# Kernel optimization log

Measured on AMD Instinct MI355X. Metric: run time of the kernel, lower is better.

## Reference

```python
import jax, jax.numpy as jnp
import numpy as np

H = 1024   # hidden_size
A = 16     # number_ab (branches)
O = 4      # num_outputs per branch
B = 4096   # batch
P = 2048   # number of selected rows
EPS = 1e-5


def setup_inputs() -> dict:
    key = jax.random.key(0)
    ks = jax.random.split(key, 12)
    s = 0.02  # weight init scale
    inp = {
        "X": jax.random.normal(ks[0], (B, H), jnp.float32),
        "X1": jax.random.normal(ks[1], (B, H), jnp.float32),
        # stacked per-branch parameters (batched over antibody axis A)
        "W1": jax.random.normal(ks[2], (A, H, H), jnp.float32) * s,
        "b1": jnp.zeros((A, H), jnp.float32),
        "W2": jax.random.normal(ks[3], (A, H, H), jnp.float32) * s,
        "b2": jnp.zeros((A, H), jnp.float32),
        "W3": jax.random.normal(ks[4], (A, H, H), jnp.float32) * s,
        "b3": jnp.zeros((A, H), jnp.float32),
        "gamma": jnp.ones((A, H), jnp.float32),
        "beta": jnp.zeros((A, H), jnp.float32),
        "W4": jax.random.normal(ks[5], (A, H, O), jnp.float32) * s,
        "b4": jnp.zeros((A, O), jnp.float32),
        "positions_y": jax.random.randint(ks[6], (P,), 0, B, jnp.int32),
    }
    return inp


def reference(X, X1, W1, b1, W2, b2, W3, b3, gamma, beta, W4, b4, positions_y):
    # z = l1(X) + l2(X1) per branch, batched over A: [B, A, H]
    z = (jnp.einsum('bh,aho->bao', X, W1) + b1
         + jnp.einsum('bh,aho->bao', X1, W2) + b2)
    # mlm: Linear -> ReLU -> LayerNorm -> Linear
    h = jax.nn.relu(jnp.einsum('bah,aho->bao', z, W3) + b3)  # [B, A, H]
    mu = jnp.mean(h, axis=-1, keepdims=True)
    var = jnp.var(h, axis=-1, keepdims=True)  # biased, matches nn.LayerNorm
    hn = (h - mu) / jnp.sqrt(var + EPS) * gamma + beta
    y = jnp.einsum('bah,aho->bao', hn, W4) + b4  # [B, A, O]
    # torch.cat along dim 1 over branches -> [B, A*O]
    Y = y.reshape(B, A * O)
    return Y[positions_y]
```

## Files before the change

### kernel.cpp

```cpp
#include <hip/hip_runtime.h>
#include <hip/hip_bf16.h>

using bf16 = __hip_bfloat16;
typedef __bf16 v8bf __attribute__((ext_vector_type(8)));
typedef float v4f __attribute__((ext_vector_type(4)));

#define H_ 1024
#define A_ 16
#define O_ 4
#define B_ 4096
#define P_ 2048
#define EPS_ 1e-5f

__device__ __forceinline__ void gl_lds16(const void* g, void* l) {
    __builtin_amdgcn_global_load_lds(
        (const __attribute__((address_space(1))) void*)g,
        (__attribute__((address_space(3))) void*)l, 16, 0, 0);
}

__global__ __launch_bounds__(256) void gather_bias_k(const float* __restrict__ X,
                                                     const float* __restrict__ X1,
                                                     const int* __restrict__ pos,
                                                     bf16* __restrict__ XX,
                                                     const float* __restrict__ b1,
                                                     const float* __restrict__ b2,
                                                     float* __restrict__ b12) {
    if (blockIdx.x >= P_) {
        int i = (blockIdx.x - P_) * 256 + threadIdx.x;
        if (i < A_ * H_) b12[i] = b1[i] + b2[i];
        return;
    }
    int p = blockIdx.x;
    int row = pos[p];
    const float4* x  = (const float4*)(X  + (size_t)row * H_);
    const float4* x1 = (const float4*)(X1 + (size_t)row * H_);
    bf16* o = XX + (size_t)p * (2 * H_);
    int i = threadIdx.x;
    float4 v = x[i];
    __align__(8) bf16 t[4];
    t[0] = __float2bfloat16(v.x); t[1] = __float2bfloat16(v.y);
    t[2] = __float2bfloat16(v.z); t[3] = __float2bfloat16(v.w);
    *(uint2*)(o + i * 4) = *(const uint2*)t;
    float4 w = x1[i];
    t[0] = __float2bfloat16(w.x); t[1] = __float2bfloat16(w.y);
    t[2] = __float2bfloat16(w.z); t[3] = __float2bfloat16(w.w);
    *(uint2*)(o + H_ + i * 4) = *(const uint2*)t;
}

__global__ __launch_bounds__(256) void transpose12_k(const float* __restrict__ W1s,
                                                     const float* __restrict__ W2s,
                                                     bf16* __restrict__ WT12) {
    __shared__ float tile[64][65];
    const int which = blockIdx.z >> 4;
    const int a = blockIdx.z & 15;
    const float* src = (which == 0) ? W1s : W2s;
    const int kOff = which * H_;

    const int k0 = blockIdx.x * 64;
    const int n0 = blockIdx.y * 64;
    const float* s = src + (size_t)a * H_ * H_;
    const int tc = threadIdx.x & 15;
    const int tr = threadIdx.x >> 4;
#pragma unroll
    for (int r = 0; r < 64; r += 16) {
        float4 v = *(const float4*)(s + (size_t)(k0 + tr + r) * H_ + n0 + tc * 4);
        tile[tr + r][tc * 4 + 0] = v.x;
        tile[tr + r][tc * 4 + 1] = v.y;
        tile[tr + r][tc * 4 + 2] = v.z;
        tile[tr + r][tc * 4 + 3] = v.w;
    }
    __syncthreads();
    bf16* d = WT12 + (size_t)a * H_ * (2 * H_) + kOff;
    const int wc = threadIdx.x & 7;
    const int wr = threadIdx.x >> 3;
#pragma unroll
    for (int r = 0; r < 64; r += 32) {
        const int n = wr + r;
        __align__(16) bf16 tmp[8];
#pragma unroll
        for (int j = 0; j < 8; j++) tmp[j] = __float2bfloat16(tile[wc * 8 + j][n]);
        *(uint4*)(d + (size_t)(n0 + n) * (2 * H_) + k0 + wc * 8) = *(const uint4*)tmp;
    }
}

template <bool RELU, bool FUSET3>
__global__ __launch_bounds__(256) void gemm_bt(const bf16* __restrict__ Amat, size_t aStrideA,
                                               const bf16* __restrict__ Bt,
                                               const float* __restrict__ bias,
                                               bf16* __restrict__ C,
                                               int M, int N, int K,
                                               const float* __restrict__ W3s,
                                               bf16* __restrict__ WT3d) {
    __shared__ __align__(16) char smem[32768];
    unsigned short* As = (unsigned short*)smem;
    unsigned short* Bs = (unsigned short*)(smem + 16384);

    const int L = blockIdx.x + 16 * blockIdx.y + 128 * blockIdx.z;

    if (FUSET3 && L >= 2048) {
        const int t = L - 2048;
        const int a = t >> 8;
        const int rem = t & 255;
        const int k0 = (rem & 15) * 64;
        const int n0 = (rem >> 4) * 64;
        float(*tile)[65] = (float(*)[65])smem;
        const float* s = W3s + (size_t)a * H_ * H_;
        const int tc = threadIdx.x & 15;
        const int tr = threadIdx.x >> 4;
#pragma unroll
        for (int r = 0; r < 64; r += 16) {
            float4 v = *(const float4*)(s + (size_t)(k0 + tr + r) * H_ + n0 + tc * 4);
            tile[tr + r][tc * 4 + 0] = v.x;
            tile[tr + r][tc * 4 + 1] = v.y;
            tile[tr + r][tc * 4 + 2] = v.z;
            tile[tr + r][tc * 4 + 3] = v.w;
        }
        __syncthreads();
        bf16* d = WT3d + (size_t)a * H_ * H_;
        const int wc = threadIdx.x & 7;
        const int wr = threadIdx.x >> 3;
#pragma unroll
        for (int r = 0; r < 64; r += 32) {
            const int n = wr + r;
            __align__(16) bf16 tmp[8];
#pragma unroll
            for (int j = 0; j < 8; j++) tmp[j] = __float2bfloat16(tile[wc * 8 + j][n]);
            *(uint4*)(d + (size_t)(n0 + n) * H_ + k0 + wc * 8) = *(const uint4*)tmp;
        }
        return;
    }

    const int xcd = L & 7;
    const int g = L >> 3;
    const int bm = g & 15;
    const int bna = xcd + 8 * (g >> 4);
    const int bn = bna & 7;
    const int a = bna >> 3;

    const bf16* Ab = Amat + (size_t)a * aStrideA;
    const bf16* Bb = Bt + (size_t)a * (size_t)N * K;
    const int tid = threadIdx.x;
    const int lane = tid & 63;
    const int wave = tid >> 6;
    const int wm = (wave & 1) * 64;
    const int wn = (wave >> 1) * 64;

    v4f acc[4][4];
#pragma unroll
    for (int i = 0; i < 4; i++)
#pragma unroll
        for (int j = 0; j < 4; j++) acc[i][j] = (v4f){0.f, 0.f, 0.f, 0.f};

    const int r0 = tid >> 2;
    const int cs = (((tid & 3) ^ ((r0 >> 1) & 3))) * 8;
    const bf16* agBase = Ab + (size_t)(bm * 128 + r0) * K + cs;
    const bf16* bgBase = Bb + (size_t)(bn * 128 + r0) * K + cs;
    const size_t rowSkip = (size_t)64 * K;
    const int w512 = wave * 512;

    const int lr = lane & 15;
    const int q = lane >> 4;
    const int kq = (q ^ ((lr >> 1) & 3)) * 8;

    const int nk = K / 32;

    gl_lds16(agBase, As + w512);
    gl_lds16(agBase + rowSkip, As + 2048 + w512);
    gl_lds16(bgBase, Bs + w512);
    gl_lds16(bgBase + rowSkip, Bs + 2048 + w512);

    for (int kt = 0; kt < nk; ++kt) {
        __syncthreads();
        if (kt + 1 < nk) {
            const int k0 = (kt + 1) * 32;
            unsigned short* aB = As + ((kt + 1) & 1) * 4096;
            unsigned short* bB = Bs + ((kt + 1) & 1) * 4096;
            gl_lds16(agBase + k0, aB + w512);
            gl_lds16(agBase + k0 + rowSkip, aB + 2048 + w512);
            gl_lds16(bgBase + k0, bB + w512);
            gl_lds16(bgBase + k0 + rowSkip, bB + 2048 + w512);
        }
        const unsigned short* Ar = As + (kt & 1) * 4096;
        const unsigned short* Br = Bs + (kt & 1) * 4096;
        v8bf af[4], bfr[4];
#pragma unroll
        for (int mi = 0; mi < 4; mi++)
            af[mi] = *(const v8bf*)(Ar + (wm + mi * 16 + lr) * 32 + kq);
#pragma unroll
        for (int ni = 0; ni < 4; ni++)
            bfr[ni] = *(const v8bf*)(Br + (wn + ni * 16 + lr) * 32 + kq);
#pragma unroll
        for (int mi = 0; mi < 4; mi++)
#pragma unroll
            for (int ni = 0; ni < 4; ni++)
                acc[mi][ni] = __builtin_amdgcn_mfma_f32_16x16x32_bf16(af[mi], bfr[ni],
                                                                      acc[mi][ni], 0, 0, 0);
    }

    const int lq = lane >> 4;
    bf16* Cb = C + (size_t)a * M * N;
#pragma unroll
    for (int ni = 0; ni < 4; ni++) {
        const int col = bn * 128 + wn + ni * 16 + lr;
        const float bv = bias[(size_t)a * N + col];
#pragma unroll
        for (int mi = 0; mi < 4; mi++) {
            const int row0 = bm * 128 + wm + mi * 16 + lq * 4;
#pragma unroll
            for (int rg = 0; rg < 4; rg++) {
                float v = acc[mi][ni][rg] + bv;
                if (RELU) v = v > 0.f ? v : 0.f;
                Cb[(size_t)(row0 + rg) * N + col] = __float2bfloat16(v);
            }
        }
    }
}

__global__ __launch_bounds__(256) void ln_head_k(const bf16* __restrict__ Hb,
                                                 const float* __restrict__ gamma,
                                                 const float* __restrict__ beta,
                                                 const float* __restrict__ W4,
                                                 const float* __restrict__ b4,
                                                 float* __restrict__ out) {
    const int w = blockIdx.x * 4 + (threadIdx.x >> 6);
    const int lane = threadIdx.x & 63;
    const int a = w >> 9;
    const int p0 = (w & 511) * 4;
    const float* g = gamma + (size_t)a * H_;
    const float* be = beta + (size_t)a * H_;
    const float4* w4 = (const float4*)(W4 + (size_t)a * H_ * O_);

    float gv[16], bv[16];
    float4 wv[16];
#pragma unroll
    for (int half = 0; half < 2; half++) {
        const int kb = half * 512 + lane * 8;
        const float4 g4a = *(const float4*)(g + kb);
        const float4 g4b = *(const float4*)(g + kb + 4);
        const float4 b4a = *(const float4*)(be + kb);
        const float4 b4b = *(const float4*)(be + kb + 4);
        gv[half * 8 + 0] = g4a.x; gv[half * 8 + 1] = g4a.y;
        gv[half * 8 + 2] = g4a.z; gv[half * 8 + 3] = g4a.w;
        gv[half * 8 + 4] = g4b.x; gv[half * 8 + 5] = g4b.y;
        gv[half * 8 + 6] = g4b.z; gv[half * 8 + 7] = g4b.w;
        bv[half * 8 + 0] = b4a.x; bv[half * 8 + 1] = b4a.y;
        bv[half * 8 + 2] = b4a.z; bv[half * 8 + 3] = b4a.w;
        bv[half * 8 + 4] = b4b.x; bv[half * 8 + 5] = b4b.y;
        bv[half * 8 + 6] = b4b.z; bv[half * 8 + 7] = b4b.w;
#pragma unroll
        for (int j = 0; j < 8; j++) wv[half * 8 + j] = w4[kb + j];
    }
    const float bo = b4[a * O_ + (lane & 3)];

    for (int rr = 0; rr < 4; rr++) {
        const int p = p0 + rr;
        const bf16* hrow = Hb + ((size_t)a * P_ + p) * H_;
        v8bf h0 = *(const v8bf*)(hrow + lane * 8);
        v8bf h1 = *(const v8bf*)(hrow + 512 + lane * 8);
        float hv[16];
        float s = 0.f, ss = 0.f;
#pragma unroll
        for (int j = 0; j < 8; j++) {
            float v = (float)h0[j];
            hv[j] = v; s += v; ss += v * v;
        }
#pragma unroll
        for (int j = 0; j < 8; j++) {
            float v = (float)h1[j];
            hv[8 + j] = v; s += v; ss += v * v;
        }
#pragma unroll
        for (int off = 32; off; off >>= 1) {
            s += __shfl_xor(s, off);
            ss += __shfl_xor(ss, off);
        }
        const float mu = s * (1.f / H_);
        const float var = ss * (1.f / H_) - mu * mu;
        const float rstd = rsqrtf(var + EPS_);
        float a0 = 0.f, a1 = 0.f, a2 = 0.f, a3 = 0.f;
#pragma unroll
        for (int j = 0; j < 16; j++) {
            const float hn = (hv[j] - mu) * rstd * gv[j] + bv[j];
            a0 += hn * wv[j].x;
            a1 += hn * wv[j].y;
            a2 += hn * wv[j].z;
            a3 += hn * wv[j].w;
        }
#pragma unroll
        for (int off = 32; off; off >>= 1) {
            a0 += __shfl_xor(a0, off);
            a1 += __shfl_xor(a1, off);
            a2 += __shfl_xor(a2, off);
            a3 += __shfl_xor(a3, off);
        }
        if (lane < 4) {
            const float v = (lane == 0 ? a0 : lane == 1 ? a1 : lane == 2 ? a2 : a3) + bo;
            out[(size_t)p * (A_ * O_) + a * O_ + lane] = v;
        }
    }
}

extern "C" void kernel_launch(void* const* d_in, const int* in_sizes, int n_in,
                              void* d_out, int out_size, void* d_ws, size_t ws_size,
                              hipStream_t stream) {
    const float* X     = (const float*)d_in[0];
    const float* X1    = (const float*)d_in[1];
    const float* W1    = (const float*)d_in[2];
    const float* b1    = (const float*)d_in[3];
    const float* W2    = (const float*)d_in[4];
    const float* b2    = (const float*)d_in[5];
    const float* W3    = (const float*)d_in[6];
    const float* b3    = (const float*)d_in[7];
    const float* gamma = (const float*)d_in[8];
    const float* beta  = (const float*)d_in[9];
    const float* W4    = (const float*)d_in[10];
    const float* b4    = (const float*)d_in[11];
    const int* pos     = (const int*)d_in[12];
    float* out = (float*)d_out;

    char* ws = (char*)d_ws;
    bf16* XX   = (bf16*)(ws);
    bf16* Z    = (bf16*)(ws + ((size_t)8 << 20));
    bf16* WT3  = (bf16*)(ws + ((size_t)72 << 20));
    bf16* WT12 = (bf16*)(ws + ((size_t)104 << 20));
    float* b12 = (float*)(ws + ((size_t)168 << 20));
    bf16* Hb   = WT12;

    gather_bias_k<<<P_ + 64, 256, 0, stream>>>(X, X1, pos, XX, b1, b2, b12);
    dim3 tgrid(H_ / 64, H_ / 64, 2 * A_);
    transpose12_k<<<tgrid, 256, 0, stream>>>(W1, W2, WT12);

    dim3 g1f(16, 8, 48);
    gemm_bt<false, true><<<g1f, 256, 0, stream>>>(XX, 0, WT12, b12, Z, P_, H_, 2 * H_,
                                                  W3, WT3);
    dim3 g2(16, 8, 16);
    gemm_bt<true, false><<<g2, 256, 0, stream>>>(Z, (size_t)P_ * H_, WT3, b3, Hb, P_, H_, H_,
                                                 nullptr, nullptr);

    ln_head_k<<<P_ * A_ / 16, 256, 0, stream>>>(Hb, gamma, beta, W4, b4, out);
}
```

Baseline: 502.1 us.

## Enlarge GEMM tiles to 256x256 with 512 threads and move W3 transpose out

The GEMM kernel now uses 256x256 output tiles per 512-thread block with a 64-wide K step and 128 KB of double-buffered LDS, which raises the arithmetic intensity of each tile load. The W3 transpose that was fused into the first GEMM's grid is moved into the standalone transpose kernel alongside W1 and W2. Bigger tiles cut global and LDS traffic per MFMA, but they give only 512 blocks and one block per CU because of the LDS size, so latency hiding may suffer. Each wave also holds 32 accumulator vectors, which raises register pressure.

```diff
diff --git a/kernel.cpp b/kernel.cpp
--- a/kernel.cpp
+++ b/kernel.cpp
@@ -47,14 +47,15 @@
     *(uint2*)(o + H_ + i * 4) = *(const uint2*)t;
 }
 
-__global__ __launch_bounds__(256) void transpose12_k(const float* __restrict__ W1s,
-                                                     const float* __restrict__ W2s,
-                                                     bf16* __restrict__ WT12) {
+__global__ __launch_bounds__(256) void transpose_k(const float* __restrict__ W1s,
+                                                   const float* __restrict__ W2s,
+                                                   const float* __restrict__ W3s,
+                                                   bf16* __restrict__ WT12,
+                                                   bf16* __restrict__ WT3) {
     __shared__ float tile[64][65];
     const int which = blockIdx.z >> 4;
     const int a = blockIdx.z & 15;
-    const float* src = (which == 0) ? W1s : W2s;
-    const int kOff = which * H_;
+    const float* src = (which == 0) ? W1s : (which == 1) ? W2s : W3s;
 
     const int k0 = blockIdx.x * 64;
     const int n0 = blockIdx.y * 64;
@@ -70,7 +71,15 @@
         tile[tr + r][tc * 4 + 3] = v.w;
     }
     __syncthreads();
-    bf16* d = WT12 + (size_t)a * H_ * (2 * H_) + kOff;
+    bf16* d;
+    int ldK;
+    if (which < 2) {
+        d = WT12 + (size_t)a * H_ * (2 * H_) + which * H_;
+        ldK = 2 * H_;
+    } else {
+        d = WT3 + (size_t)a * H_ * H_;
+        ldK = H_;
+    }
     const int wc = threadIdx.x & 7;
     const int wr = threadIdx.x >> 3;
 #pragma unroll
@@ -79,133 +88,121 @@
         __align__(16) bf16 tmp[8];
 #pragma unroll
         for (int j = 0; j < 8; j++) tmp[j] = __float2bfloat16(tile[wc * 8 + j][n]);
-        *(uint4*)(d + (size_t)(n0 + n) * (2 * H_) + k0 + wc * 8) = *(const uint4*)tmp;
-    }
-}
-
-template <bool RELU, bool FUSET3>
-__global__ __launch_bounds__(256) void gemm_bt(const bf16* __restrict__ Amat, size_t aStrideA,
+        *(uint4*)(d + (size_t)(n0 + n) * ldK + k0 + wc * 8) = *(const uint4*)tmp;
+    }
+}
+
+template <bool RELU>
+__global__ __launch_bounds__(512) void gemm_bt(const bf16* __restrict__ Amat, size_t aStrideA,
                                                const bf16* __restrict__ Bt,
                                                const float* __restrict__ bias,
                                                bf16* __restrict__ C,
-                                               int M, int N, int K,
-                                               const float* __restrict__ W3s,
-                                               bf16* __restrict__ WT3d) {
-    __shared__ __align__(16) char smem[32768];
-    unsigned short* As = (unsigned short*)smem;
-    unsigned short* Bs = (unsigned short*)(smem + 16384);
-
-    const int L = blockIdx.x + 16 * blockIdx.y + 128 * blockIdx.z;
-
-    if (FUSET3 && L >= 2048) {
-        const int t = L - 2048;
-        const int a = t >> 8;
-        const int rem = t & 255;
-        const int k0 = (rem & 15) * 64;
-        const int n0 = (rem >> 4) * 64;
-        float(*tile)[65] = (float(*)[65])smem;
-        const float* s = W3s + (size_t)a * H_ * H_;
-        const int tc = threadIdx.x & 15;
-        const int tr = threadIdx.x >> 4;
-#pragma unroll
-        for (int r = 0; r < 64; r += 16) {
-            float4 v = *(const float4*)(s + (size_t)(k0 + tr + r) * H_ + n0 + tc * 4);
-            tile[tr + r][tc * 4 + 0] = v.x;
-            tile[tr + r][tc * 4 + 1] = v.y;
-            tile[tr + r][tc * 4 + 2] = v.z;
-            tile[tr + r][tc * 4 + 3] = v.w;
-        }
-        __syncthreads();
-        bf16* d = WT3d + (size_t)a * H_ * H_;
-        const int wc = threadIdx.x & 7;
-        const int wr = threadIdx.x >> 3;
-#pragma unroll
-        for (int r = 0; r < 64; r += 32) {
-            const int n = wr + r;
-            __align__(16) bf16 tmp[8];
-#pragma unroll
-            for (int j = 0; j < 8; j++) tmp[j] = __float2bfloat16(tile[wc * 8 + j][n]);
-            *(uint4*)(d + (size_t)(n0 + n) * H_ + k0 + wc * 8) = *(const uint4*)tmp;
-        }
-        return;
-    }
-
+                                               int M, int N, int K) {
+    __shared__ __align__(16) char smem[131072];
+
+    const int L = blockIdx.x;
     const int xcd = L & 7;
     const int g = L >> 3;
-    const int bm = g & 15;
-    const int bna = xcd + 8 * (g >> 4);
-    const int bn = bna & 7;
-    const int a = bna >> 3;
+    const int bm = g & 7;
+    const int bna = xcd + 8 * (g >> 3);
+    const int bn = bna & 3;
+    const int a = bna >> 2;
 
     const bf16* Ab = Amat + (size_t)a * aStrideA;
     const bf16* Bb = Bt + (size_t)a * (size_t)N * K;
+
     const int tid = threadIdx.x;
     const int lane = tid & 63;
-    const int wave = tid >> 6;
-    const int wm = (wave & 1) * 64;
-    const int wn = (wave >> 1) * 64;
-
-    v4f acc[4][4];
-#pragma unroll
-    for (int i = 0; i < 4; i++)
-#pragma unroll
-        for (int j = 0; j < 4; j++) acc[i][j] = (v4f){0.f, 0.f, 0.f, 0.f};
-
-    const int r0 = tid >> 2;
-    const int cs = (((tid & 3) ^ ((r0 >> 1) & 3))) * 8;
-    const bf16* agBase = Ab + (size_t)(bm * 128 + r0) * K + cs;
-    const bf16* bgBase = Bb + (size_t)(bn * 128 + r0) * K + cs;
-    const size_t rowSkip = (size_t)64 * K;
-    const int w512 = wave * 512;
-
+    const int w = tid >> 6;
     const int lr = lane & 15;
     const int q = lane >> 4;
-    const int kq = (q ^ ((lr >> 1) & 3)) * 8;
-
-    const int nk = K / 32;
-
-    gl_lds16(agBase, As + w512);
-    gl_lds16(agBase + rowSkip, As + 2048 + w512);
-    gl_lds16(bgBase, Bs + w512);
-    gl_lds16(bgBase + rowSkip, Bs + 2048 + w512);
-
-    for (int kt = 0; kt < nk; ++kt) {
+    const int wm = (w >> 2) * 128;
+    const int wn = (w & 3) * 64;
+
+    const int swz = lr & 7;
+    const int aRd0 = (wm + lr) * 128 + ((q ^ swz) << 4);
+    const int aRd1 = (wm + lr) * 128 + (((q + 4) ^ swz) << 4);
+    const int bRd0 = (wn + lr) * 128 + ((q ^ swz) << 4);
+    const int bRd1 = (wn + lr) * 128 + (((q + 4) ^ swz) << 4);
+
+    const int sr = lane >> 3;
+    const int sc = (lane & 7) ^ sr;
+    const size_t k8 = (size_t)8 * K;
+    const bf16* aSt = Ab + (size_t)(bm * 256 + w * 32 + sr) * K + sc * 8;
+    const bf16* bSt = Bb + (size_t)(bn * 256 + w * 32 + sr) * K + sc * 8;
+    char* AsL = smem + w * 4096;
+    char* BsL = smem + 65536 + w * 4096;
+
+    v4f acc[8][4];
+#pragma unroll
+    for (int i = 0; i < 8; i++)
+#pragma unroll
+        for (int j = 0; j < 4; j++) acc[i][j] = (v4f){0.f, 0.f, 0.f, 0.f};
+
+    const int nk = K / 64;
+
+#define STAGE(tt, bo)                                    \
+    {                                                    \
+        const bf16* as_ = aSt + (size_t)(tt) * 64;       \
+        const bf16* bs_ = bSt + (size_t)(tt) * 64;       \
+        gl_lds16(as_,            AsL + (bo));            \
+        gl_lds16(as_ + k8,       AsL + (bo) + 1024);     \
+        gl_lds16(as_ + 2 * k8,   AsL + (bo) + 2048);     \
+        gl_lds16(as_ + 3 * k8,   AsL + (bo) + 3072);     \
+        gl_lds16(bs_,            BsL + (bo));            \
+        gl_lds16(bs_ + k8,       BsL + (bo) + 1024);     \
+        gl_lds16(bs_ + 2 * k8,   BsL + (bo) + 2048);     \
+        gl_lds16(bs_ + 3 * k8,   BsL + (bo) + 3072);     \
+    }
+
+    STAGE(0, 0);
+
+    for (int t = 0; t < nk; ++t) {
+        const int bo = (t & 1) << 15;
+        asm volatile("s_waitcnt vmcnt(0)" ::: "memory");
         __syncthreads();
-        if (kt + 1 < nk) {
-            const int k0 = (kt + 1) * 32;
-            unsigned short* aB = As + ((kt + 1) & 1) * 4096;
-            unsigned short* bB = Bs + ((kt + 1) & 1) * 4096;
-            gl_lds16(agBase + k0, aB + w512);
-            gl_lds16(agBase + k0 + rowSkip, aB + 2048 + w512);
-            gl_lds16(bgBase + k0, bB + w512);
-            gl_lds16(bgBase + k0 + rowSkip, bB + 2048 + w512);
-        }
-        const unsigned short* Ar = As + (kt & 1) * 4096;
-        const unsigned short* Br = Bs + (kt & 1) * 4096;
-        v8bf af[4], bfr[4];
-#pragma unroll
-        for (int mi = 0; mi < 4; mi++)
-            af[mi] = *(const v8bf*)(Ar + (wm + mi * 16 + lr) * 32 + kq);
-#pragma unroll
-        for (int ni = 0; ni < 4; ni++)
-            bfr[ni] = *(const v8bf*)(Br + (wn + ni * 16 + lr) * 32 + kq);
-#pragma unroll
-        for (int mi = 0; mi < 4; mi++)
-#pragma unroll
-            for (int ni = 0; ni < 4; ni++)
-                acc[mi][ni] = __builtin_amdgcn_mfma_f32_16x16x32_bf16(af[mi], bfr[ni],
-                                                                      acc[mi][ni], 0, 0, 0);
-    }
-
-    const int lq = lane >> 4;
-    bf16* Cb = C + (size_t)a * M * N;
+        if (t + 1 < nk) STAGE(t + 1, bo ^ 32768);
+
+        const char* Ar = smem + bo;
+        const char* Br = smem + 65536 + bo;
+
+        {
+            v8bf a0[8], b0[4];
+#pragma unroll
+            for (int ni = 0; ni < 4; ni++) b0[ni] = *(const v8bf*)(Br + bRd0 + ni * 2048);
+#pragma unroll
+            for (int mi = 0; mi < 8; mi++) a0[mi] = *(const v8bf*)(Ar + aRd0 + mi * 2048);
+#pragma unroll
+            for (int mi = 0; mi < 8; mi++)
+#pragma unroll
+                for (int ni = 0; ni < 4; ni++)
+                    acc[mi][ni] = __builtin_amdgcn_mfma_f32_16x16x32_bf16(a0[mi], b0[ni],
+                                                                          acc[mi][ni], 0, 0, 0);
+        }
+        {
+            v8bf a1[8], b1[4];
+#pragma unroll
+            for (int ni = 0; ni < 4; ni++) b1[ni] = *(const v8bf*)(Br + bRd1 + ni * 2048);
+#pragma unroll
+            for (int mi = 0; mi < 8; mi++) a1[mi] = *(const v8bf*)(Ar + aRd1 + mi * 2048);
+#pragma unroll
+            for (int mi = 0; mi < 8; mi++)
+#pragma unroll
+                for (int ni = 0; ni < 4; ni++)
+                    acc[mi][ni] = __builtin_amdgcn_mfma_f32_16x16x32_bf16(a1[mi], b1[ni],
+                                                                          acc[mi][ni], 0, 0, 0);
+        }
+    }
+#undef STAGE
+
+    bf16* Cb = C + (size_t)a * (size_t)M * N;
 #pragma unroll
     for (int ni = 0; ni < 4; ni++) {
-        const int col = bn * 128 + wn + ni * 16 + lr;
+        const int col = bn * 256 + wn + ni * 16 + lr;
         const float bv = bias[(size_t)a * N + col];
 #pragma unroll
-        for (int mi = 0; mi < 4; mi++) {
-            const int row0 = bm * 128 + wm + mi * 16 + lq * 4;
+        for (int mi = 0; mi < 8; mi++) {
+            const int row0 = bm * 256 + wm + mi * 16 + q * 4;
 #pragma unroll
             for (int rg = 0; rg < 4; rg++) {
                 float v = acc[mi][ni][rg] + bv;
@@ -327,15 +324,11 @@
     bf16* Hb   = WT12;
 
     gather_bias_k<<<P_ + 64, 256, 0, stream>>>(X, X1, pos, XX, b1, b2, b12);
-    dim3 tgrid(H_ / 64, H_ / 64, 2 * A_);
-    transpose12_k<<<tgrid, 256, 0, stream>>>(W1, W2, WT12);
-
-    dim3 g1f(16, 8, 48);
-    gemm_bt<false, true><<<g1f, 256, 0, stream>>>(XX, 0, WT12, b12, Z, P_, H_, 2 * H_,
-                                                  W3, WT3);
-    dim3 g2(16, 8, 16);
-    gemm_bt<true, false><<<g2, 256, 0, stream>>>(Z, (size_t)P_ * H_, WT3, b3, Hb, P_, H_, H_,
-                                                 nullptr, nullptr);
+    dim3 tgrid(H_ / 64, H_ / 64, 3 * A_);
+    transpose_k<<<tgrid, 256, 0, stream>>>(W1, W2, W3, WT12, WT3);
+
+    gemm_bt<false><<<512, 512, 0, stream>>>(XX, 0, WT12, b12, Z, P_, H_, 2 * H_);
+    gemm_bt<true><<<512, 512, 0, stream>>>(Z, (size_t)P_ * H_, WT3, b3, Hb, P_, H_, H_);
 
     ln_head_k<<<P_ * A_ / 16, 256, 0, stream>>>(Hb, gamma, beta, W4, b4, out);
 }
```

Result: faster. 463.1 us (-7.8%).
